# Optimization experiments

Hardware: AMD Instinct MI355X
Metric: run time of the kernel (lower is better)

## Reference

```python
import jax, jax.numpy as jnp
import numpy as np

OUT = 14          # output_size of mask_roi_pool
RATIO = 2         # sampling_ratio
SCALES = (0.25, 0.125, 0.0625, 0.03125)  # strides 4,8,16,32 for 800x800 images
CANON_SCALE = 224.0
CANON_LVL = 4.0
K_MIN = 2.0       # -log2(0.25)
K_MAX = 5.0


def setup_inputs() -> dict:
    key = jax.random.key(0)
    ks = jax.random.split(key, 8)
    B, N, C = 2, 128, 256
    feats = {}
    for i, hw in enumerate([200, 100, 50, 25]):
        feats[f"feat{i}"] = jax.random.normal(ks[i], (B, C, hw, hw), dtype=jnp.float32)
    # valid xyxy boxes in [0,800] with log-uniform sizes spanning all FPN levels
    img = 800.0
    logw = jax.random.uniform(ks[4], (B, N), minval=jnp.log(16.0), maxval=jnp.log(600.0))
    logh = jax.random.uniform(ks[5], (B, N), minval=jnp.log(16.0), maxval=jnp.log(600.0))
    w, h = jnp.exp(logw), jnp.exp(logh)
    x1 = jax.random.uniform(ks[6], (B, N)) * (img - w)
    y1 = jax.random.uniform(ks[7], (B, N)) * (img - h)
    boxes = jnp.stack([x1, y1, x1 + w, y1 + h], axis=-1).astype(jnp.float32)
    feats["boxes"] = boxes
    return feats


def _prep_axis(c, L):
    # torchvision roi_align bilinear clamp semantics (aligned=False)
    valid = (c > -1.0) & (c < L)
    c = jnp.clip(c, 0.0, L - 1.0)
    lo = jnp.clip(jnp.floor(c), 0.0, L - 2.0).astype(jnp.int32)
    frac = c - lo.astype(c.dtype)
    return valid, lo, frac


def _roi_align_level(feat, rois, bidx, scale):
    # feat: [B,C,H,W], rois: [K,4] xyxy image coords, bidx: [K] int32
    B, C, H, W = feat.shape
    K = rois.shape[0]
    x1 = rois[:, 0] * scale
    y1 = rois[:, 1] * scale
    x2 = rois[:, 2] * scale
    y2 = rois[:, 3] * scale
    rw = jnp.maximum(x2 - x1, 1.0)
    rh = jnp.maximum(y2 - y1, 1.0)
    bw = rw / OUT
    bh = rh / OUT
    # sample offsets within roi in bin units: (ph*RATIO + iy + 0.5)/RATIO, flattened [OUT*RATIO]
    off = (jnp.arange(OUT * RATIO, dtype=feat.dtype) + 0.5) / RATIO
    ys = y1[:, None] + bh[:, None] * off  # [K, 28]
    xs = x1[:, None] + bw[:, None] * off  # [K, 28]
    vy, ylo, ly = _prep_axis(ys, H)
    vx, xlo, lx = _prep_axis(xs, W)
    hy, hx = 1.0 - ly, 1.0 - lx
    feat_r = feat.transpose(0, 2, 3, 1).reshape(B * H * W, C)
    base = bidx[:, None, None] * (H * W)

    def gather(yi, xi):
        idx = base + yi[:, :, None] * W + xi[:, None, :]  # [K,28,28]
        return feat_r[idx]  # [K,28,28,C]

    val = (gather(ylo, xlo) * (hy[:, :, None] * hx[:, None, :])[..., None]
           + gather(ylo, xlo + 1) * (hy[:, :, None] * lx[:, None, :])[..., None]
           + gather(ylo + 1, xlo) * (ly[:, :, None] * hx[:, None, :])[..., None]
           + gather(ylo + 1, xlo + 1) * (ly[:, :, None] * lx[:, None, :])[..., None])
    mask = (vy[:, :, None] & vx[:, None, :])[..., None]
    val = jnp.where(mask, val, 0.0)
    # average RATIO x RATIO samples per output bin
    val = val.reshape(K, OUT, RATIO, OUT, RATIO, C).mean(axis=(2, 4))
    return val.transpose(0, 3, 1, 2)  # [K, C, OUT, OUT]


def _forward(feat0, feat1, feat2, feat3, boxes):
    feats = (feat0, feat1, feat2, feat3)
    B, N = boxes.shape[0], boxes.shape[1]
    rois = boxes.reshape(B * N, 4)
    bidx = jnp.repeat(jnp.arange(B, dtype=jnp.int32), N)
    # FPN level mapper (torchvision LevelMapper)
    w = rois[:, 2] - rois[:, 0]
    h = rois[:, 3] - rois[:, 1]
    s = jnp.sqrt(w * h)
    lvl = jnp.floor(CANON_LVL + jnp.log2(s / CANON_SCALE + 1e-6))
    lvl_idx = (jnp.clip(lvl, K_MIN, K_MAX) - K_MIN).astype(jnp.int32)  # [K] in 0..3
    per_level = jnp.stack(
        [_roi_align_level(f, rois, bidx, sc) for f, sc in zip(feats, SCALES)]
    )  # [4, K, C, 14, 14]
    K = rois.shape[0]
    return per_level[lvl_idx, jnp.arange(K)]  # [K, C, 14, 14]


def reference(feat0, feat1, feat2, feat3, boxes):
    return _forward(feat0, feat1, feat2, feat3, boxes)
```

## Files before the change

kernel.cpp:

```cpp
#include <hip/hip_runtime.h>
#include <math.h>

#define OUT 14
#define RATIO 2
#define NS (OUT*RATIO)
#define NPIX (OUT*OUT)
#define C_TOT 256
#define CG 4
#define GPB 4
#define NCHUNK (C_TOT/(CG*GPB))
#define NBOX_PER_B 128
#define NTHREADS 256
#define PATCH_CAP 1280
#define MAXIT 5
#define NROI 256

__device__ __forceinline__ void prep_axis(float c, int L, int& lo, float& fh, float& fl)
{
    const bool  v  = (c > -1.0f) && (c < (float)L);
    const float cc = fminf(fmaxf(c, 0.0f), (float)(L - 1));
    const float fb = fminf(fmaxf(floorf(cc), 0.0f), (float)(L - 2));
    const float fr = cc - fb;
    lo = (int)fb;
    fl = v ? fr        : 0.0f;
    fh = v ? 1.0f - fr : 0.0f;
}

__device__ __forceinline__ int axis_lo(float c, int L)
{
    const float cc = fminf(fmaxf(c, 0.0f), (float)(L - 1));
    return (int)fminf(fmaxf(floorf(cc), 0.0f), (float)(L - 2));
}

__global__ __launch_bounds__(NTHREADS)
void roi_align_fused4_kernel(const float* __restrict__ f0,
                             const float* __restrict__ f1,
                             const float* __restrict__ f2,
                             const float* __restrict__ f3,
                             const float* __restrict__ boxes,
                             float* __restrict__ out)
{
    const int chunk = blockIdx.x;
    const int k     = blockIdx.y;
    const int tid   = threadIdx.x;

    __shared__ float4 s_patch[PATCH_CAP];

    const float bx1 = boxes[k*4+0];
    const float by1 = boxes[k*4+1];
    const float bx2 = boxes[k*4+2];
    const float by2 = boxes[k*4+3];

    const float wbox = bx2 - bx1;
    const float hbox = by2 - by1;
    const float sdim = sqrtf(wbox * hbox);
    float lvlf = floorf(4.0f + log2f(sdim / 224.0f + 1e-6f));
    lvlf = fminf(fmaxf(lvlf, 2.0f), 5.0f);
    const int lidx = (int)lvlf - 2;

    const float* fptr;
    int H, W;
    float scale;
    if      (lidx == 0) { fptr = f0; H = 200; W = 200; scale = 0.25f;    }
    else if (lidx == 1) { fptr = f1; H = 100; W = 100; scale = 0.125f;   }
    else if (lidx == 2) { fptr = f2; H = 50;  W = 50;  scale = 0.0625f;  }
    else                { fptr = f3; H = 25;  W = 25;  scale = 0.03125f; }

    const float x1 = bx1 * scale;
    const float y1 = by1 * scale;
    const float x2 = bx2 * scale;
    const float y2 = by2 * scale;
    const float rw = fmaxf(x2 - x1, 1.0f);
    const float rh = fmaxf(y2 - y1, 1.0f);
    const float bw = rw / (float)OUT;
    const float bh = rh / (float)OUT;

    const float off0  = 0.25f;
    const float offL  = ((float)(NS-1) + 0.5f) * 0.5f;
    const int ymin  = axis_lo(y1 + bh * off0, H);
    const int xmin  = axis_lo(x1 + bw * off0, W);
    const int nrows = axis_lo(y1 + bh * offL, H) + 2 - ymin;
    const int ncols = axis_lo(x1 + bw * offL, W) + 2 - xmin;
    const int padded  = ncols | 1;
    const int stridep = (nrows * padded <= PATCH_CAP) ? padded : ncols;
    const int nelem   = nrows * ncols;
    const float rcpc  = 1.0f / (float)ncols;

    const bool active = (tid < NPIX);
    int rb0 = 0, rb1 = 0, cb0 = 0, cb1 = 0;
    float4 wy = {0,0,0,0};
    float4 wx = {0,0,0,0};
    if (active) {
        const int ph = tid / OUT;
        const int pw = tid - ph * OUT;
        int lo; float fh, fl;
        prep_axis(y1 + bh * (((float)(2*ph)   + 0.5f) * 0.5f), H, lo, fh, fl);
        rb0 = (lo - ymin) * stridep; wy.x = fh * 0.25f; wy.y = fl * 0.25f;
        prep_axis(y1 + bh * (((float)(2*ph+1) + 0.5f) * 0.5f), H, lo, fh, fl);
        rb1 = (lo - ymin) * stridep; wy.z = fh * 0.25f; wy.w = fl * 0.25f;
        prep_axis(x1 + bw * (((float)(2*pw)   + 0.5f) * 0.5f), W, lo, fh, fl);
        cb0 = lo - xmin; wx.x = fh; wx.y = fl;
        prep_axis(x1 + bw * (((float)(2*pw+1) + 0.5f) * 0.5f), W, lo, fh, fl);
        cb1 = lo - xmin; wx.z = fh; wx.w = fl;
    }

    const size_t plane = (size_t)H * (size_t)W;
    int go_[MAXIT], di_[MAXIT];
    #pragma unroll
    for (int t = 0; t < MAXIT; ++t) {
        const int i  = t*NTHREADS + tid;
        const int r  = (int)(((float)i + 0.5f) * rcpc);
        const int cc = i - r * ncols;
        go_[t] = r * W + cc;
        di_[t] = (i < nelem && r * stridep + cc < PATCH_CAP) ? (r * stridep + cc) : -1;
    }

    const float* fbase = fptr
        + ((size_t)(k / NBOX_PER_B) * C_TOT + (size_t)chunk * (GPB*CG)) * plane
        + (size_t)ymin * W + xmin;
    float* outk = out + ((size_t)k * C_TOT + (size_t)chunk * (GPB*CG)) * NPIX;

    #pragma unroll
    for (int g = 0; g < GPB; ++g) {
        const float* g0 = fbase + (size_t)(g*CG) * plane;
        const float* g1 = g0 +   plane;
        const float* g2 = g0 + 2*plane;
        const float* g3 = g0 + 3*plane;
        #pragma unroll
        for (int t = 0; t < MAXIT; ++t) {
            if (di_[t] >= 0) {
                const int go = go_[t];
                float4 v;
                v.x = g0[go]; v.y = g1[go]; v.z = g2[go]; v.w = g3[go];
                s_patch[di_[t]] = v;
            }
        }
        __syncthreads();

        if (active) {
            float4 acc = {0.0f, 0.0f, 0.0f, 0.0f};
            #pragma unroll
            for (int ys = 0; ys < 2; ++ys) {
                const int   rb = ys ? rb1 : rb0;
                const float yh = ys ? wy.z : wy.x;
                const float yl = ys ? wy.w : wy.y;
                #pragma unroll
                for (int xs = 0; xs < 2; ++xs) {
                    const int base = rb + (xs ? cb1 : cb0);
                    const float xh = xs ? wx.z : wx.x;
                    const float xl = xs ? wx.w : wx.y;
                    const float w00 = yh*xh, w01 = yh*xl, w10 = yl*xh, w11 = yl*xl;
                    const float4 v00 = s_patch[base];
                    const float4 v01 = s_patch[base + 1];
                    const float4 v10 = s_patch[base + stridep];
                    const float4 v11 = s_patch[base + stridep + 1];
                    acc.x += w00*v00.x + w01*v01.x + w10*v10.x + w11*v11.x;
                    acc.y += w00*v00.y + w01*v01.y + w10*v10.y + w11*v11.y;
                    acc.z += w00*v00.z + w01*v01.z + w10*v10.z + w11*v11.z;
                    acc.w += w00*v00.w + w01*v01.w + w10*v10.w + w11*v11.w;
                }
            }
            float* ob = outk + (size_t)(g*CG) * NPIX + tid;
            ob[0*NPIX] = acc.x;
            ob[1*NPIX] = acc.y;
            ob[2*NPIX] = acc.z;
            ob[3*NPIX] = acc.w;
        }
        if (g + 1 < GPB) __syncthreads();
    }
}

extern "C" void kernel_launch(void* const* d_in, const int* in_sizes, int n_in,
                              void* d_out, int out_size, void* d_ws, size_t ws_size,
                              hipStream_t stream) {
    const float* f0    = (const float*)d_in[0];
    const float* f1    = (const float*)d_in[1];
    const float* f2    = (const float*)d_in[2];
    const float* f3    = (const float*)d_in[3];
    const float* boxes = (const float*)d_in[4];
    float* out = (float*)d_out;

    dim3 grid(NCHUNK, NROI);
    roi_align_fused4_kernel<<<grid, NTHREADS, 0, stream>>>(f0, f1, f2, f3, boxes, out);
}
```

Measured before the change: 37.30 us.

## Process channel groups in pairs with double-size shared patch to use idle threads

The kernel now loads two 4-channel groups into a doubled shared-memory patch per phase, so each phase covers 8 channels and only two barrier rounds are needed instead of four. The 392 pixel-tasks per phase are spread across all 256 threads, with the first 136 threads taking a second pixel, which removes the 60 idle threads of the old 196-pixel mapping. In exchange, shared memory use doubles to 40 KB per block, which can lower occupancy, and threads hold more loads in flight and more registers.

```diff
diff --git a/kernel.cpp b/kernel.cpp
--- a/kernel.cpp
+++ b/kernel.cpp
@@ -14,6 +14,8 @@
 #define PATCH_CAP 1280
 #define MAXIT 5
 #define NROI 256
+#define NTASK (2*NPIX)
+#define NB (NTASK - NTHREADS)
 
 __device__ __forceinline__ void prep_axis(float c, int L, int& lo, float& fh, float& fl)
 {
@@ -32,8 +34,56 @@
     return (int)fminf(fmaxf(floorf(cc), 0.0f), (float)(L - 2));
 }
 
+struct PixPrep { int rb0, rb1, cb0, cb1; float4 wy, wx; };
+
+__device__ __forceinline__ PixPrep make_prep(int px, float y1, float bh, float x1, float bw,
+                                             int H, int W, int ymin, int xmin, int stridep)
+{
+    PixPrep p;
+    const int ph = px / OUT;
+    const int pw = px - ph * OUT;
+    int lo; float fh, fl;
+    prep_axis(y1 + bh * (((float)(2*ph)   + 0.5f) * 0.5f), H, lo, fh, fl);
+    p.rb0 = (lo - ymin) * stridep; p.wy.x = fh * 0.25f; p.wy.y = fl * 0.25f;
+    prep_axis(y1 + bh * (((float)(2*ph+1) + 0.5f) * 0.5f), H, lo, fh, fl);
+    p.rb1 = (lo - ymin) * stridep; p.wy.z = fh * 0.25f; p.wy.w = fl * 0.25f;
+    prep_axis(x1 + bw * (((float)(2*pw)   + 0.5f) * 0.5f), W, lo, fh, fl);
+    p.cb0 = lo - xmin; p.wx.x = fh; p.wx.y = fl;
+    prep_axis(x1 + bw * (((float)(2*pw+1) + 0.5f) * 0.5f), W, lo, fh, fl);
+    p.cb1 = lo - xmin; p.wx.z = fh; p.wx.w = fl;
+    return p;
+}
+
+__device__ __forceinline__ float4 bilin16(const float4* __restrict__ sp,
+                                          const PixPrep& p, int stridep)
+{
+    float4 acc = {0.0f, 0.0f, 0.0f, 0.0f};
+    #pragma unroll
+    for (int ys = 0; ys < 2; ++ys) {
+        const int   rb = ys ? p.rb1 : p.rb0;
+        const float yh = ys ? p.wy.z : p.wy.x;
+        const float yl = ys ? p.wy.w : p.wy.y;
+        #pragma unroll
+        for (int xs = 0; xs < 2; ++xs) {
+            const int base = rb + (xs ? p.cb1 : p.cb0);
+            const float xh = xs ? p.wx.z : p.wx.x;
+            const float xl = xs ? p.wx.w : p.wx.y;
+            const float w00 = yh*xh, w01 = yh*xl, w10 = yl*xh, w11 = yl*xl;
+            const float4 v00 = sp[base];
+            const float4 v01 = sp[base + 1];
+            const float4 v10 = sp[base + stridep];
+            const float4 v11 = sp[base + stridep + 1];
+            acc.x += w00*v00.x + w01*v01.x + w10*v10.x + w11*v11.x;
+            acc.y += w00*v00.y + w01*v01.y + w10*v10.y + w11*v11.y;
+            acc.z += w00*v00.z + w01*v01.z + w10*v10.z + w11*v11.z;
+            acc.w += w00*v00.w + w01*v01.w + w10*v10.w + w11*v11.w;
+        }
+    }
+    return acc;
+}
+
 __global__ __launch_bounds__(NTHREADS)
-void roi_align_fused4_kernel(const float* __restrict__ f0,
+void roi_align_fusedp_kernel(const float* __restrict__ f0,
                              const float* __restrict__ f1,
                              const float* __restrict__ f2,
                              const float* __restrict__ f3,
@@ -44,7 +94,7 @@
     const int k     = blockIdx.y;
     const int tid   = threadIdx.x;
 
-    __shared__ float4 s_patch[PATCH_CAP];
+    __shared__ float4 s_patch[2*PATCH_CAP];
 
     const float bx1 = boxes[k*4+0];
     const float by1 = boxes[k*4+1];
@@ -86,23 +136,14 @@
     const int nelem   = nrows * ncols;
     const float rcpc  = 1.0f / (float)ncols;
 
-    const bool active = (tid < NPIX);
-    int rb0 = 0, rb1 = 0, cb0 = 0, cb1 = 0;
-    float4 wy = {0,0,0,0};
-    float4 wx = {0,0,0,0};
-    if (active) {
-        const int ph = tid / OUT;
-        const int pw = tid - ph * OUT;
-        int lo; float fh, fl;
-        prep_axis(y1 + bh * (((float)(2*ph)   + 0.5f) * 0.5f), H, lo, fh, fl);
-        rb0 = (lo - ymin) * stridep; wy.x = fh * 0.25f; wy.y = fl * 0.25f;
-        prep_axis(y1 + bh * (((float)(2*ph+1) + 0.5f) * 0.5f), H, lo, fh, fl);
-        rb1 = (lo - ymin) * stridep; wy.z = fh * 0.25f; wy.w = fl * 0.25f;
-        prep_axis(x1 + bw * (((float)(2*pw)   + 0.5f) * 0.5f), W, lo, fh, fl);
-        cb0 = lo - xmin; wx.x = fh; wx.y = fl;
-        prep_axis(x1 + bw * (((float)(2*pw+1) + 0.5f) * 0.5f), W, lo, fh, fl);
-        cb1 = lo - xmin; wx.z = fh; wx.w = fl;
-    }
+    const int  pxA = (tid < NPIX) ? tid : tid - NPIX;
+    const bool hiA = (tid >= NPIX);
+    const bool actB = (tid < NB);
+    const int  pxB = tid + (NPIX - NB);
+
+    const PixPrep prA = make_prep(pxA, y1, bh, x1, bw, H, W, ymin, xmin, stridep);
+    PixPrep prB;
+    if (actB) prB = make_prep(pxB, y1, bh, x1, bw, H, W, ymin, xmin, stridep);
 
     const size_t plane = (size_t)H * (size_t)W;
     int go_[MAXIT], di_[MAXIT];
@@ -111,8 +152,9 @@
         const int i  = t*NTHREADS + tid;
         const int r  = (int)(((float)i + 0.5f) * rcpc);
         const int cc = i - r * ncols;
+        const int di = r * stridep + cc;
         go_[t] = r * W + cc;
-        di_[t] = (i < nelem && r * stridep + cc < PATCH_CAP) ? (r * stridep + cc) : -1;
+        di_[t] = (i < nelem && di < PATCH_CAP) ? di : -1;
     }
 
     const float* fbase = fptr
@@ -121,52 +163,45 @@
     float* outk = out + ((size_t)k * C_TOT + (size_t)chunk * (GPB*CG)) * NPIX;
 
     #pragma unroll
-    for (int g = 0; g < GPB; ++g) {
-        const float* g0 = fbase + (size_t)(g*CG) * plane;
-        const float* g1 = g0 +   plane;
-        const float* g2 = g0 + 2*plane;
-        const float* g3 = g0 + 3*plane;
+    for (int pair = 0; pair < 2; ++pair) {
+        const float* a0 = fbase + (size_t)((2*pair)  *CG) * plane;
+        const float* b0 = fbase + (size_t)((2*pair+1)*CG) * plane;
         #pragma unroll
         for (int t = 0; t < MAXIT; ++t) {
             if (di_[t] >= 0) {
                 const int go = go_[t];
-                float4 v;
-                v.x = g0[go]; v.y = g1[go]; v.z = g2[go]; v.w = g3[go];
-                s_patch[di_[t]] = v;
+                float4 va, vb;
+                va.x = a0[go];         vb.x = b0[go];
+                va.y = a0[go+plane];   vb.y = b0[go+plane];
+                va.z = a0[go+2*plane]; vb.z = b0[go+2*plane];
+                va.w = a0[go+3*plane]; vb.w = b0[go+3*plane];
+                s_patch[di_[t]]             = va;
+                s_patch[di_[t] + PATCH_CAP] = vb;
             }
         }
         __syncthreads();
 
-        if (active) {
-            float4 acc = {0.0f, 0.0f, 0.0f, 0.0f};
-            #pragma unroll
-            for (int ys = 0; ys < 2; ++ys) {
-                const int   rb = ys ? rb1 : rb0;
-                const float yh = ys ? wy.z : wy.x;
-                const float yl = ys ? wy.w : wy.y;
-                #pragma unroll
-                for (int xs = 0; xs < 2; ++xs) {
-                    const int base = rb + (xs ? cb1 : cb0);
-                    const float xh = xs ? wx.z : wx.x;
-                    const float xl = xs ? wx.w : wx.y;
-                    const float w00 = yh*xh, w01 = yh*xl, w10 = yl*xh, w11 = yl*xl;
-                    const float4 v00 = s_patch[base];
-                    const float4 v01 = s_patch[base + 1];
-                    const float4 v10 = s_patch[base + stridep];
-                    const float4 v11 = s_patch[base + stridep + 1];
-                    acc.x += w00*v00.x + w01*v01.x + w10*v10.x + w11*v11.x;
-                    acc.y += w00*v00.y + w01*v01.y + w10*v10.y + w11*v11.y;
-                    acc.z += w00*v00.z + w01*v01.z + w10*v10.z + w11*v11.z;
-                    acc.w += w00*v00.w + w01*v01.w + w10*v10.w + w11*v11.w;
-                }
-            }
-            float* ob = outk + (size_t)(g*CG) * NPIX + tid;
+        {
+            const float4* sp = s_patch + (hiA ? PATCH_CAP : 0);
+            const float4 acc = bilin16(sp, prA, stridep);
+            const int lg = 2*pair + (hiA ? 1 : 0);
+            float* ob = outk + (size_t)(lg*CG) * NPIX + pxA;
             ob[0*NPIX] = acc.x;
             ob[1*NPIX] = acc.y;
             ob[2*NPIX] = acc.z;
             ob[3*NPIX] = acc.w;
         }
-        if (g + 1 < GPB) __syncthreads();
+        if (actB) {
+            const float4* sp = s_patch + PATCH_CAP;
+            const float4 acc = bilin16(sp, prB, stridep);
+            const int lg = 2*pair + 1;
+            float* ob = outk + (size_t)(lg*CG) * NPIX + pxB;
+            ob[0*NPIX] = acc.x;
+            ob[1*NPIX] = acc.y;
+            ob[2*NPIX] = acc.z;
+            ob[3*NPIX] = acc.w;
+        }
+        if (pair == 0) __syncthreads();
     }
 }
 
@@ -181,5 +216,5 @@
     float* out = (float*)d_out;
 
     dim3 grid(NCHUNK, NROI);
-    roi_align_fused4_kernel<<<grid, NTHREADS, 0, stream>>>(f0, f1, f2, f3, boxes, out);
-}
+    roi_align_fusedp_kernel<<<grid, NTHREADS, 0, stream>>>(f0, f1, f2, f3, boxes, out);
+}
```

New measurement: 38.34 us. 1.03x slower.
